# Performance work log

Measured on AMD Instinct MI355X. Metric: run time of the kernel, lower is better.

Reference implementation:

```python
import jax, jax.numpy as jnp
import numpy as np

H, DQK, DV, DM, POS = 8, 64, 64, 768, 64

def _rel_basis(l, n):
    # Enformer central-mask relative position basis: [l, l, n]
    pos = jnp.arange(l)
    distance = pos[None, :] - pos[:, None]              # [l, l] int
    half = n // 2
    pow_rate = jnp.exp(jnp.log(jnp.asarray((l + 1) / 2.0, jnp.float32)) / half)
    center_widths = pow_rate ** jnp.arange(1, half + 1, dtype=jnp.float32)  # [half]
    unsigned = (jnp.abs(distance)[:, :, None].astype(jnp.float32) <= center_widths)
    signed = jnp.sign(distance)[:, :, None] * unsigned
    return jnp.concatenate([unsigned.astype(jnp.float32), signed.astype(jnp.float32)], axis=-1)

def setup_inputs() -> dict:
    key = jax.random.key(0)
    ks = jax.random.split(key, 9)
    b, l = 2, 1024
    x = jax.random.normal(ks[0], (b, l, DM), jnp.float32)
    # torch Linear weights: [out, in]
    Wq = jax.random.normal(ks[1], (H * DQK, DM), jnp.float32) * (1.0 / np.sqrt(DM))
    Wk = jax.random.normal(ks[2], (H * DQK, DM), jnp.float32) * (1.0 / np.sqrt(DM))
    Wv = jax.random.normal(ks[3], (H * DV, DM), jnp.float32) * (1.0 / np.sqrt(DM))
    Wo = jax.random.normal(ks[4], (DM, H * DV), jnp.float32) * (1.0 / np.sqrt(H * DV))
    bo = jnp.zeros((DM,), jnp.float32)
    u_bias = jax.random.normal(ks[5], (H, DQK), jnp.float32) * np.sqrt(2.0 / DQK)
    v_bias = jax.random.normal(ks[6], (H, DQK), jnp.float32) * np.sqrt(2.0 / DQK)
    w_pos = jax.random.normal(ks[7], (H, DQK, POS), jnp.float32) * np.sqrt(2.0 / POS)
    return {"x": x, "Wq": Wq, "Wk": Wk, "Wv": Wv, "Wo": Wo, "bo": bo,
            "u_bias": u_bias, "v_bias": v_bias, "w_pos": w_pos}

def reference(x, Wq, Wk, Wv, Wo, bo, u_bias, v_bias, w_pos):
    b, l, _ = x.shape
    q = (x @ Wq.T).reshape(b, l, H, DQK)
    k = (x @ Wk.T).reshape(b, l, H, DQK)
    v = (x @ Wv.T).reshape(b, l, H, DV)
    basis = _rel_basis(l, POS)                           # [l, l, n]
    scale = 1.0 / np.sqrt(DQK)
    # qr_term: einsum('bihd,hdn,ijn->bhij') factored to avoid [b,h,l,l,d]
    qw = jnp.einsum('bihd,hdn->bhin', q, w_pos)          # [b,h,l,n]
    qr = jnp.einsum('bhin,ijn->bhij', qw, basis)
    uk = jnp.einsum('hd,bjhd->bhj', u_bias, k)[:, :, None, :]
    vw = jnp.einsum('hd,hdn->hn', v_bias, w_pos)
    vr = jnp.einsum('hn,ijn->hij', vw, basis)[None]      # [1,h,l,l]
    bias = (qr + uk + vr) * scale
    scores = jnp.einsum('bihd,bjhd->bhij', q, k) * scale + bias
    attn = jax.nn.softmax(scores, axis=-1)
    out = jnp.einsum('bhij,bjhd->bihd', attn, v).reshape(b, l, H * DV)
    return out @ Wo.T + bo
```

## Files before the change

kernel.cpp:

```cpp
#include <hip/hip_runtime.h>
#include <hip/hip_bf16.h>

#define LSEQ 1024
#define NB   2
#define NH   8
#define DD   64
#define DMOD 768

using bf16x8 = __attribute__((ext_vector_type(8))) short;
using f32x4  = __attribute__((ext_vector_type(4))) float;

__device__ inline unsigned short f2bf(float f) {
    union { float f; unsigned u; } v; v.f = f;
    unsigned r = v.u + 0x7FFFu + ((v.u >> 16) & 1u);
    return (unsigned short)(r >> 16);
}
__device__ inline unsigned pk2bf(float a, float b) {
    union { __hip_bfloat162 h; unsigned u; } c;
    c.h = __float22bfloat162_rn(make_float2(a, b));
    return c.u;
}

__global__ __launch_bounds__(256) void gemm_qkv(
    const float* __restrict__ X,
    const float* __restrict__ Wq, const float* __restrict__ Wk,
    const float* __restrict__ Wv,
    const float* __restrict__ u_bias, const float* __restrict__ v_bias,
    const float* __restrict__ w_pos,
    unsigned short* __restrict__ Qb, unsigned short* __restrict__ Kb,
    unsigned short* __restrict__ Vtb,
    float* __restrict__ wsfx, unsigned char* __restrict__ cls_g)
{
    int tid = threadIdx.x;

    if (blockIdx.y == 32) {
        int sb = blockIdx.x;
        if (sb == 0) {
            __shared__ float w_s[32];
            __shared__ int cmin_s[1024];
            if (tid < 32) {
                float pr = expf(logf(512.5f) / 32.0f);
                w_s[tid] = powf(pr, (float)(tid + 1));
            }
            __syncthreads();
            for (int d = tid; d < 1024; d += 256) {
                float fd = (float)d;
                int cm = 32;
                for (int c = 31; c >= 0; --c) if (fd <= w_s[c]) cm = c;
                cmin_s[d] = cm;
            }
            __syncthreads();
            for (int d2 = tid; d2 < 2048; d2 += 256) {
                int dd = d2 - 1023;
                int ad = dd < 0 ? -dd : dd; if (ad > 1023) ad = 1023;
                int t = (dd < 0) ? 0 : ((dd == 0) ? 1 : 2);
                cls_g[d2] = (unsigned char)(t * 33 + cmin_s[ad]);
            }
        } else if (sb <= 8) {
            int h = sb - 1;
            __shared__ float vred[4][64];
            __shared__ float ured[4][64];
            __shared__ float wd[64];
            int n = tid & 63, g = tid >> 6;
            float vs = 0.f, us = 0.f;
#pragma unroll
            for (int k = 0; k < 16; ++k) {
                int d = g * 16 + k;
                float wp = w_pos[(h * 64 + d) * 64 + n];
                vs += v_bias[h * 64 + d] * wp;
                us += u_bias[h * 64 + d] * wp;
            }
            vred[g][n] = vs; ured[g][n] = us;
            __syncthreads();
            if (tid < 64) {
                float v4 = vred[0][tid] + vred[1][tid] + vred[2][tid] + vred[3][tid];
                float u4 = ured[0][tid] + ured[1][tid] + ured[2][tid] + ured[3][tid];
                wd[tid] = v4 - u4;
            }
            __syncthreads();
            if (tid < 64) {
                int nn = tid & 31, cb = tid & 32;
                float s = 0.f;
                for (int c = 31; c >= nn; --c) s += wd[cb + c];
                wsfx[h * 64 + tid] = s * 0.125f;
            }
        }
        return;
    }

    __shared__ unsigned short Xs[64][40];
    __shared__ unsigned short Wsm[64][40];
    __shared__ unsigned short Ct[64][72];

    int w = tid >> 6, lane = tid & 63, l15 = lane & 15, q = lane >> 4;
    int M0 = blockIdx.y * 64, N0 = blockIdx.x * 64;
    int rs = tid >> 2, seg = tid & 3;

    const float* Wsrc; int Nrow;
    if (N0 < 512)       { Wsrc = Wq; Nrow = N0; }
    else if (N0 < 1024) { Wsrc = Wk; Nrow = N0 - 512; }
    else                { Wsrc = Wv; Nrow = N0 - 1024; }

    const float* xrow = X    + (size_t)(M0 + rs) * 768 + seg * 8;
    const float* wrow = Wsrc + (size_t)(Nrow + rs) * 768 + seg * 8;

    f32x4 acc[4] = {};
    for (int k0 = 0; k0 < 768; k0 += 32) {
        float4 xa = *(const float4*)(xrow + k0);
        float4 xb = *(const float4*)(xrow + k0 + 4);
        float4 wa = *(const float4*)(wrow + k0);
        float4 wb = *(const float4*)(wrow + k0 + 4);
        uint4 xp, wp;
        xp.x = pk2bf(xa.x, xa.y); xp.y = pk2bf(xa.z, xa.w);
        xp.z = pk2bf(xb.x, xb.y); xp.w = pk2bf(xb.z, xb.w);
        wp.x = pk2bf(wa.x, wa.y); wp.y = pk2bf(wa.z, wa.w);
        wp.z = pk2bf(wb.x, wb.y); wp.w = pk2bf(wb.z, wb.w);
        *(uint4*)&Xs[rs][seg * 8]  = xp;
        *(uint4*)&Wsm[rs][seg * 8] = wp;
        __syncthreads();
        bf16x8 a = *(bf16x8*)&Xs[w * 16 + l15][q * 8];
#pragma unroll
        for (int ct = 0; ct < 4; ++ct) {
            bf16x8 bfr = *(bf16x8*)&Wsm[ct * 16 + l15][q * 8];
            acc[ct] = __builtin_amdgcn_mfma_f32_16x16x32_bf16(a, bfr, acc[ct], 0, 0, 0);
        }
        __syncthreads();
    }

    if (N0 < 1024) {
        int isQ = (N0 < 512);
#pragma unroll
        for (int ct = 0; ct < 4; ++ct) {
            float u0 = isQ ? u_bias[N0 + ct * 16 + l15] : 0.f;
            float sc = isQ ? 0.125f : 1.0f;
#pragma unroll
            for (int r = 0; r < 4; ++r)
                Ct[w * 16 + q * 4 + r][ct * 16 + l15] = f2bf((acc[ct][r] + u0) * sc);
        }
        __syncthreads();
        int Nh = isQ ? N0 : (N0 - 512);
        unsigned short* out = isQ ? Qb : Kb;
        size_t base = ((size_t)((M0 >> 10) * 8 + (Nh >> 6)) * 1024 + (M0 & 1023)) * 64;
#pragma unroll
        for (int it = 0; it < 2; ++it) {
            int idx = tid + it * 256;
            int row = idx >> 3, sg = idx & 7;
            *(uint4*)(out + base + (size_t)row * 64 + sg * 8) = *(uint4*)&Ct[row][sg * 8];
        }
    } else {
#pragma unroll
        for (int ct = 0; ct < 4; ++ct) {
            ushort4 pk;
            pk.x = f2bf(acc[ct][0]); pk.y = f2bf(acc[ct][1]);
            pk.z = f2bf(acc[ct][2]); pk.w = f2bf(acc[ct][3]);
            *(ushort4*)&Ct[ct * 16 + l15][w * 16 + q * 4] = pk;
        }
        __syncthreads();
        size_t base = ((size_t)((M0 >> 10) * 8 + ((N0 - 1024) >> 6))) * 65536;
        int j0 = M0 & 1023;
#pragma unroll
        for (int it = 0; it < 2; ++it) {
            int idx = tid + it * 256;
            int d = idx >> 3, sg = idx & 7;
            *(uint4*)(Vtb + base + (size_t)d * 1024 + j0 + sg * 8) = *(uint4*)&Ct[d][sg * 8];
        }
    }
}

__global__ __launch_bounds__(256) void gemm_o(
    const unsigned short* __restrict__ X, const float* __restrict__ W,
    const float* __restrict__ bias, float* __restrict__ out)
{
    __shared__ unsigned short Xs[64][40];
    __shared__ unsigned short Wsm[64][40];
    __shared__ float Ctf[64][72];

    int tid = threadIdx.x;
    int w = tid >> 6, lane = tid & 63, l15 = lane & 15, q = lane >> 4;
    int M0 = blockIdx.y * 64, N0 = blockIdx.x * 64;
    int rs = tid >> 2, seg = tid & 3;

    const float* wrow = W + (size_t)(N0 + rs) * 512 + seg * 8;

    f32x4 acc[4] = {};
    for (int k0 = 0; k0 < 512; k0 += 32) {
        uint4 xv = *(const uint4*)(X + (size_t)(M0 + rs) * 512 + k0 + seg * 8);
        float4 wa = *(const float4*)(wrow + k0);
        float4 wb = *(const float4*)(wrow + k0 + 4);
        uint4 wp;
        wp.x = pk2bf(wa.x, wa.y); wp.y = pk2bf(wa.z, wa.w);
        wp.z = pk2bf(wb.x, wb.y); wp.w = pk2bf(wb.z, wb.w);
        *(uint4*)&Xs[rs][seg * 8]  = xv;
        *(uint4*)&Wsm[rs][seg * 8] = wp;
        __syncthreads();
        bf16x8 a = *(bf16x8*)&Xs[w * 16 + l15][q * 8];
#pragma unroll
        for (int ct = 0; ct < 4; ++ct) {
            bf16x8 bfr = *(bf16x8*)&Wsm[ct * 16 + l15][q * 8];
            acc[ct] = __builtin_amdgcn_mfma_f32_16x16x32_bf16(a, bfr, acc[ct], 0, 0, 0);
        }
        __syncthreads();
    }
#pragma unroll
    for (int ct = 0; ct < 4; ++ct) {
        float bv = bias[N0 + ct * 16 + l15];
#pragma unroll
        for (int r = 0; r < 4; ++r)
            Ctf[w * 16 + q * 4 + r][ct * 16 + l15] = acc[ct][r] + bv;
    }
    __syncthreads();
#pragma unroll
    for (int it = 0; it < 4; ++it) {
        int idx = tid + it * 256;
        int row = idx >> 4, sg = idx & 15;
        *(float4*)(out + (size_t)(M0 + row) * 768 + N0 + sg * 4) = *(float4*)&Ctf[row][sg * 4];
    }
}

__global__ __launch_bounds__(256, 4) void attn_mfma(
    const unsigned short* __restrict__ Qbf,
    const unsigned short* __restrict__ Kbf,
    const unsigned short* __restrict__ Vt,
    const float* __restrict__ w_pos,
    const float* __restrict__ wsfx,
    const unsigned char* __restrict__ cls_g,
    unsigned short* __restrict__ ao)
{
    __shared__ float biasT[16 * 99];
    __shared__ unsigned char cls[2048];
    __shared__ unsigned short Pl[4][16][76];
    union Ovl {
        struct { unsigned short wptS[64][68]; float qwL[16][68]; } pre;
        struct { float Obuf[4][64][17]; float lbuf[4][16]; } post;
    };
    __shared__ Ovl ovl;

    int tid = threadIdx.x;
    int b = blockIdx.z, h = blockIdx.y, bh = b * 8 + h;
    int i0 = blockIdx.x * 16;
    int w = tid >> 6, lane = tid & 63, l15 = lane & 15, q = lane >> 4;

    for (int idx = tid; idx < 512; idx += 256)
        ((unsigned int*)cls)[idx] = ((const unsigned int*)cls_g)[idx];
    {
        const float4* wsrc = (const float4*)(w_pos + h * 4096);
#pragma unroll
        for (int it = 0; it < 4; ++it) {
            int f = tid + it * 256;
            float4 wv = wsrc[f];
            int d = f >> 4, n4 = (f & 15) * 4;
            ovl.pre.wptS[n4 + 0][d] = f2bf(wv.x);
            ovl.pre.wptS[n4 + 1][d] = f2bf(wv.y);
            ovl.pre.wptS[n4 + 2][d] = f2bf(wv.z);
            ovl.pre.wptS[n4 + 3][d] = f2bf(wv.w);
        }
    }

    int ig = i0 + l15;
    const unsigned short* qrow = Qbf + ((size_t)bh * 1024 + ig) * 64;
    bf16x8 qf0 = *(const bf16x8*)(qrow + q * 8);
    bf16x8 qf1 = *(const bf16x8*)(qrow + 32 + q * 8);
    __syncthreads();

    {
        bf16x8 b0 = *(bf16x8*)&ovl.pre.wptS[w * 16 + l15][q * 8];
        bf16x8 b1 = *(bf16x8*)&ovl.pre.wptS[w * 16 + l15][32 + q * 8];
        f32x4 a = {};
        a = __builtin_amdgcn_mfma_f32_16x16x32_bf16(qf0, b0, a, 0, 0, 0);
        a = __builtin_amdgcn_mfma_f32_16x16x32_bf16(qf1, b1, a, 0, 0, 0);
#pragma unroll
        for (int r = 0; r < 4; ++r)
            ovl.pre.qwL[q * 4 + r][w * 16 + l15] = a[r];
    }
    __syncthreads();

    const float* wsh = wsfx + h * 64;
#pragma unroll
    for (int it = 0; it < 4; ++it) {
        int idx = tid + it * 256;
        int il = idx >> 6, n = idx & 63, nn = n & 31, cb = n & 32;
        float run = 0.f, s = 0.f;
#pragma unroll
        for (int c = 31; c >= 0; --c) {
            run += ovl.pre.qwL[il][cb + c];
            if (c == nn) s = run;
        }
        ovl.pre.qwL[il][n] = s + wsh[n];
    }
    __syncthreads();

    for (int idx = tid; idx < 528; idx += 256) {
        int il = idx / 33, c = idx - il * 33;
        float up = 0.f, sp = 0.f;
        if (c < 32) {
            up = ovl.pre.qwL[il][c];
            sp = ovl.pre.qwL[il][32 + c];
        }
        float* bt = biasT + il * 99;
        bt[c]      = up - sp;
        bt[33 + c] = up;
        bt[66 + c] = up + sp;
    }
    __syncthreads();

    const unsigned short* Kbase = Kbf + (size_t)bh * 65536;
    const unsigned short* Vbase = Vt  + (size_t)bh * 65536;
    const float* btrow = biasT + l15 * 99;
    int clsoff = 1023 - ig;

    f32x4 Oacc[4] = {};
    float lsum = 0.f;

    for (int jt = 0; jt < 4; ++jt) {
        int jb = w * 256 + jt * 64;
        f32x4 st[4];
#pragma unroll
        for (int ct = 0; ct < 4; ++ct) {
            const unsigned short* krow = Kbase + (size_t)(jb + ct * 16 + l15) * 64;
            bf16x8 ka0 = *(const bf16x8*)(krow + q * 8);
            bf16x8 ka1 = *(const bf16x8*)(krow + 32 + q * 8);
            f32x4 a = {};
            a = __builtin_amdgcn_mfma_f32_16x16x32_bf16(ka0, qf0, a, 0, 0, 0);
            a = __builtin_amdgcn_mfma_f32_16x16x32_bf16(ka1, qf1, a, 0, 0, 0);
            st[ct] = a;
        }
#pragma unroll
        for (int ct = 0; ct < 4; ++ct) {
            int d2b = jb + ct * 16 + q * 4 + clsoff;
            float pv[4];
#pragma unroll
            for (int r = 0; r < 4; ++r) {
                float s = st[ct][r] + btrow[cls[d2b + r]];
                float p = __expf(s);
                lsum += p;
                pv[r] = p;
            }
            ushort4 pk;
            pk.x = f2bf(pv[0]); pk.y = f2bf(pv[1]);
            pk.z = f2bf(pv[2]); pk.w = f2bf(pv[3]);
            *(ushort4*)&Pl[w][l15][ct * 16 + q * 4] = pk;
        }
#pragma unroll
        for (int ks = 0; ks < 2; ++ks) {
            bf16x8 pb = *(const bf16x8*)&Pl[w][l15][ks * 32 + q * 8];
#pragma unroll
            for (int dt = 0; dt < 4; ++dt) {
                bf16x8 va = *(const bf16x8*)(Vbase + (size_t)(dt * 16 + l15) * 1024
                                             + jb + ks * 32 + q * 8);
                Oacc[dt] = __builtin_amdgcn_mfma_f32_16x16x32_bf16(va, pb, Oacc[dt], 0, 0, 0);
            }
        }
    }

    lsum += __shfl_xor(lsum, 16);
    lsum += __shfl_xor(lsum, 32);

    __syncthreads();
#pragma unroll
    for (int dt = 0; dt < 4; ++dt)
#pragma unroll
        for (int r = 0; r < 4; ++r)
            ovl.post.Obuf[w][dt * 16 + q * 4 + r][l15] = Oacc[dt][r];
    if (lane < 16) ovl.post.lbuf[w][l15] = lsum;
    __syncthreads();

    for (int t2 = tid; t2 < 1024; t2 += 256) {
        int il = t2 >> 6, d = t2 & 63;
        float o = ovl.post.Obuf[0][d][il] + ovl.post.Obuf[1][d][il]
                + ovl.post.Obuf[2][d][il] + ovl.post.Obuf[3][d][il];
        float l = ovl.post.lbuf[0][il] + ovl.post.lbuf[1][il]
                + ovl.post.lbuf[2][il] + ovl.post.lbuf[3][il];
        ao[((size_t)(b * 1024 + i0 + il)) * 512 + h * 64 + d] = f2bf(o / l);
    }
}

extern "C" void kernel_launch(void* const* d_in, const int* in_sizes, int n_in,
                              void* d_out, int out_size, void* d_ws, size_t ws_size,
                              hipStream_t stream)
{
    const float* x      = (const float*)d_in[0];
    const float* Wq     = (const float*)d_in[1];
    const float* Wk     = (const float*)d_in[2];
    const float* Wv     = (const float*)d_in[3];
    const float* Wo     = (const float*)d_in[4];
    const float* bo     = (const float*)d_in[5];
    const float* u_bias = (const float*)d_in[6];
    const float* v_bias = (const float*)d_in[7];
    const float* w_pos  = (const float*)d_in[8];
    float* out = (float*)d_out;

    char* ws = (char*)d_ws;
    unsigned short* Qbf  = (unsigned short*)ws;            ws += 2097152;
    unsigned short* Kbf  = (unsigned short*)ws;            ws += 2097152;
    unsigned short* Vtb  = (unsigned short*)ws;            ws += 2097152;
    unsigned short* aob  = (unsigned short*)ws;            ws += 2097152;
    float*          wsfx = (float*)ws;                     ws += 2048;
    unsigned char*  clsg = (unsigned char*)ws;             ws += 2048;

    gemm_qkv<<<dim3(24, 33), 256, 0, stream>>>(
        x, Wq, Wk, Wv, u_bias, v_bias, w_pos,
        Qbf, Kbf, Vtb, wsfx, clsg);

    attn_mfma<<<dim3(64, 8, 2), 256, 0, stream>>>(
        Qbf, Kbf, Vtb, w_pos, wsfx, clsg, aob);

    gemm_o<<<dim3(12, 32), 256, 0, stream>>>(aob, Wo, bo, out);
}
```

Baseline: 138.8 us.

## Double-buffer LDS tiles in projection GEMMs and halve output GEMM M-tile

Both projection GEMMs now use two LDS buffers. Global loads for the next K slice are issued before the MFMAs on the current slice, and only one barrier runs per step, so load latency overlaps with compute. The output GEMM tile shrinks to 32 rows, giving twice as many blocks (12x64) so the few blocks in that launch fill the GPU better, with each wave computing a 16x32 sub-tile. The attention jt loop is also fully unrolled, which may raise register pressure.

```diff
diff --git a/kernel.cpp b/kernel.cpp
--- a/kernel.cpp
+++ b/kernel.cpp
@@ -88,8 +88,8 @@
         return;
     }
 
-    __shared__ unsigned short Xs[64][40];
-    __shared__ unsigned short Wsm[64][40];
+    __shared__ unsigned short Xs[2][64][40];
+    __shared__ unsigned short Wsm[2][64][40];
     __shared__ unsigned short Ct[64][72];
 
     int w = tid >> 6, lane = tid & 63, l15 = lane & 15, q = lane >> 4;
@@ -104,25 +104,46 @@
     const float* xrow = X    + (size_t)(M0 + rs) * 768 + seg * 8;
     const float* wrow = Wsrc + (size_t)(Nrow + rs) * 768 + seg * 8;
 
-    f32x4 acc[4] = {};
-    for (int k0 = 0; k0 < 768; k0 += 32) {
-        float4 xa = *(const float4*)(xrow + k0);
-        float4 xb = *(const float4*)(xrow + k0 + 4);
-        float4 wa = *(const float4*)(wrow + k0);
-        float4 wb = *(const float4*)(wrow + k0 + 4);
+    {
+        float4 xa = *(const float4*)(xrow);
+        float4 xb = *(const float4*)(xrow + 4);
+        float4 wa = *(const float4*)(wrow);
+        float4 wb = *(const float4*)(wrow + 4);
         uint4 xp, wp;
         xp.x = pk2bf(xa.x, xa.y); xp.y = pk2bf(xa.z, xa.w);
         xp.z = pk2bf(xb.x, xb.y); xp.w = pk2bf(xb.z, xb.w);
         wp.x = pk2bf(wa.x, wa.y); wp.y = pk2bf(wa.z, wa.w);
         wp.z = pk2bf(wb.x, wb.y); wp.w = pk2bf(wb.z, wb.w);
-        *(uint4*)&Xs[rs][seg * 8]  = xp;
-        *(uint4*)&Wsm[rs][seg * 8] = wp;
-        __syncthreads();
-        bf16x8 a = *(bf16x8*)&Xs[w * 16 + l15][q * 8];
+        *(uint4*)&Xs[0][rs][seg * 8]  = xp;
+        *(uint4*)&Wsm[0][rs][seg * 8] = wp;
+    }
+    __syncthreads();
+
+    f32x4 acc[4] = {};
+    for (int step = 0; step < 24; ++step) {
+        int cur = step & 1;
+        float4 xa, xb, wa, wb;
+        if (step < 23) {
+            int k0 = (step + 1) * 32;
+            xa = *(const float4*)(xrow + k0);
+            xb = *(const float4*)(xrow + k0 + 4);
+            wa = *(const float4*)(wrow + k0);
+            wb = *(const float4*)(wrow + k0 + 4);
+        }
+        bf16x8 a = *(bf16x8*)&Xs[cur][w * 16 + l15][q * 8];
 #pragma unroll
         for (int ct = 0; ct < 4; ++ct) {
-            bf16x8 bfr = *(bf16x8*)&Wsm[ct * 16 + l15][q * 8];
+            bf16x8 bfr = *(bf16x8*)&Wsm[cur][ct * 16 + l15][q * 8];
             acc[ct] = __builtin_amdgcn_mfma_f32_16x16x32_bf16(a, bfr, acc[ct], 0, 0, 0);
+        }
+        if (step < 23) {
+            uint4 xp, wp;
+            xp.x = pk2bf(xa.x, xa.y); xp.y = pk2bf(xa.z, xa.w);
+            xp.z = pk2bf(xb.x, xb.y); xp.w = pk2bf(xb.z, xb.w);
+            wp.x = pk2bf(wa.x, wa.y); wp.y = pk2bf(wa.z, wa.w);
+            wp.z = pk2bf(wb.x, wb.y); wp.w = pk2bf(wb.z, wb.w);
+            *(uint4*)&Xs[cur ^ 1][rs][seg * 8]  = xp;
+            *(uint4*)&Wsm[cur ^ 1][rs][seg * 8] = wp;
         }
         __syncthreads();
     }
@@ -171,46 +192,69 @@
     const unsigned short* __restrict__ X, const float* __restrict__ W,
     const float* __restrict__ bias, float* __restrict__ out)
 {
-    __shared__ unsigned short Xs[64][40];
-    __shared__ unsigned short Wsm[64][40];
-    __shared__ float Ctf[64][72];
+    __shared__ unsigned short Xs[2][32][40];
+    __shared__ unsigned short Wsm[2][64][40];
+    __shared__ float Ctf[32][72];
 
     int tid = threadIdx.x;
     int w = tid >> 6, lane = tid & 63, l15 = lane & 15, q = lane >> 4;
-    int M0 = blockIdx.y * 64, N0 = blockIdx.x * 64;
-    int rs = tid >> 2, seg = tid & 3;
-
-    const float* wrow = W + (size_t)(N0 + rs) * 512 + seg * 8;
-
-    f32x4 acc[4] = {};
-    for (int k0 = 0; k0 < 512; k0 += 32) {
-        uint4 xv = *(const uint4*)(X + (size_t)(M0 + rs) * 512 + k0 + seg * 8);
-        float4 wa = *(const float4*)(wrow + k0);
-        float4 wb = *(const float4*)(wrow + k0 + 4);
+    int mh = w & 1, nh = w >> 1;
+    int M0 = blockIdx.y * 32, N0 = blockIdx.x * 64;
+
+    int xr = tid >> 3, xseg = tid & 7;
+    int wr = tid >> 2, wseg = tid & 3;
+
+    const unsigned short* xrow = X + (size_t)(M0 + xr) * 512 + xseg * 4;
+    const float*          wrow = W + (size_t)(N0 + wr) * 512 + wseg * 8;
+
+    {
+        ushort4 xv = *(const ushort4*)(xrow);
+        float4 wa = *(const float4*)(wrow);
+        float4 wb = *(const float4*)(wrow + 4);
         uint4 wp;
         wp.x = pk2bf(wa.x, wa.y); wp.y = pk2bf(wa.z, wa.w);
         wp.z = pk2bf(wb.x, wb.y); wp.w = pk2bf(wb.z, wb.w);
-        *(uint4*)&Xs[rs][seg * 8]  = xv;
-        *(uint4*)&Wsm[rs][seg * 8] = wp;
+        *(ushort4*)&Xs[0][xr][xseg * 4] = xv;
+        *(uint4*)&Wsm[0][wr][wseg * 8]  = wp;
+    }
+    __syncthreads();
+
+    f32x4 acc[2] = {};
+    for (int step = 0; step < 16; ++step) {
+        int cur = step & 1;
+        ushort4 xv; float4 wa, wb;
+        if (step < 15) {
+            int k0 = (step + 1) * 32;
+            xv = *(const ushort4*)(xrow + k0);
+            wa = *(const float4*)(wrow + k0);
+            wb = *(const float4*)(wrow + k0 + 4);
+        }
+        bf16x8 a = *(bf16x8*)&Xs[cur][mh * 16 + l15][q * 8];
+#pragma unroll
+        for (int ct = 0; ct < 2; ++ct) {
+            bf16x8 bfr = *(bf16x8*)&Wsm[cur][nh * 32 + ct * 16 + l15][q * 8];
+            acc[ct] = __builtin_amdgcn_mfma_f32_16x16x32_bf16(a, bfr, acc[ct], 0, 0, 0);
+        }
+        if (step < 15) {
+            uint4 wp;
+            wp.x = pk2bf(wa.x, wa.y); wp.y = pk2bf(wa.z, wa.w);
+            wp.z = pk2bf(wb.x, wb.y); wp.w = pk2bf(wb.z, wb.w);
+            *(ushort4*)&Xs[cur ^ 1][xr][xseg * 4] = xv;
+            *(uint4*)&Wsm[cur ^ 1][wr][wseg * 8]  = wp;
+        }
         __syncthreads();
-        bf16x8 a = *(bf16x8*)&Xs[w * 16 + l15][q * 8];
-#pragma unroll
-        for (int ct = 0; ct < 4; ++ct) {
-            bf16x8 bfr = *(bf16x8*)&Wsm[ct * 16 + l15][q * 8];
-            acc[ct] = __builtin_amdgcn_mfma_f32_16x16x32_bf16(a, bfr, acc[ct], 0, 0, 0);
-        }
-        __syncthreads();
-    }
-#pragma unroll
-    for (int ct = 0; ct < 4; ++ct) {
-        float bv = bias[N0 + ct * 16 + l15];
+    }
+
+#pragma unroll
+    for (int ct = 0; ct < 2; ++ct) {
+        float bv = bias[N0 + nh * 32 + ct * 16 + l15];
 #pragma unroll
         for (int r = 0; r < 4; ++r)
-            Ctf[w * 16 + q * 4 + r][ct * 16 + l15] = acc[ct][r] + bv;
-    }
-    __syncthreads();
-#pragma unroll
-    for (int it = 0; it < 4; ++it) {
+            Ctf[mh * 16 + q * 4 + r][nh * 32 + ct * 16 + l15] = acc[ct][r] + bv;
+    }
+    __syncthreads();
+#pragma unroll
+    for (int it = 0; it < 2; ++it) {
         int idx = tid + it * 256;
         int row = idx >> 4, sg = idx & 15;
         *(float4*)(out + (size_t)(M0 + row) * 768 + N0 + sg * 4) = *(float4*)&Ctf[row][sg * 4];
@@ -311,6 +355,7 @@
     f32x4 Oacc[4] = {};
     float lsum = 0.f;
 
+#pragma unroll
     for (int jt = 0; jt < 4; ++jt) {
         int jb = w * 256 + jt * 64;
         f32x4 st[4];
@@ -404,5 +449,5 @@
     attn_mfma<<<dim3(64, 8, 2), 256, 0, stream>>>(
         Qbf, Kbf, Vtb, w_pos, wsfx, clsg, aob);
 
-    gemm_o<<<dim3(12, 32), 256, 0, stream>>>(aob, Wo, bo, out);
-}
+    gemm_o<<<dim3(12, 64), 256, 0, stream>>>(aob, Wo, bo, out);
+}
```

Result: no change. 137.9 us (-0.6%).
